# Kernel optimization log

Hardware: AMD Instinct MI355X
Metric: run time of the kernel (lower is better)

## Reference

```python
import jax, jax.numpy as jnp
import numpy as np

M_RANGE = 3
K = 2 * M_RANGE + 1          # kernel size = 7
N_CLASS = K * K              # 49 motion classes
IM_CHANNEL = 3


def setup_inputs() -> dict:
    key = jax.random.key(0)
    k1, k2, k3, k4 = jax.random.split(key, 4)
    B, H, W = 16, 256, 256
    im_input = jax.random.normal(k1, (B, 2 * IM_CHANNEL, H, W), dtype=jnp.float32)
    im_output = jax.random.normal(k2, (B, IM_CHANNEL, H, W), dtype=jnp.float32)
    # motion in [-M_RANGE, M_RANGE-1) so that floor(m)+M_RANGE+1 <= K-1 (valid bin)
    gt_motion = jax.random.uniform(k3, (B, 2, H, W), dtype=jnp.float32) * (2 * M_RANGE - 1) - M_RANGE
    # grouped-conv weight (already in post-swapaxes [n_class, 1, K, K] layout)
    m_kernel = jax.random.uniform(k4, (N_CLASS, 1, K, K), dtype=jnp.float32)
    return {"im_input": im_input, "im_output": im_output,
            "gt_motion": gt_motion, "m_kernel": m_kernel}


def _axis_weights(m):
    # m: [B,H,W] -> bilinear binning weights over K bins: [B,H,W,K]
    f = jnp.floor(m)
    frac = m - f
    idx = f.astype(jnp.int32) + M_RANGE
    oh0 = jax.nn.one_hot(idx, K, dtype=m.dtype)
    oh1 = jax.nn.one_hot(idx + 1, K, dtype=m.dtype)
    return (1.0 - frac)[..., None] * oh0 + frac[..., None] * oh1


def motion2mask(motion):
    # faithful vectorization of the triple-loop: mask[c=iy*K+ix] = b[iy]*a[ix]
    ax = _axis_weights(motion[:, 0])   # x-motion -> columns of ger(b, a)
    ay = _axis_weights(motion[:, 1])   # y-motion -> rows
    mask = ay[..., :, None] * ax[..., None, :]       # [B,H,W,K,K] outer product
    B, H, W = motion.shape[0], motion.shape[2], motion.shape[3]
    return mask.reshape(B, H, W, N_CLASS).transpose(0, 3, 1, 2)  # [B,N_CLASS,H,W]


def _conv(x, w, groups):
    return jax.lax.conv_general_dilated(
        x, w, window_strides=(1, 1),
        padding=[(M_RANGE, M_RANGE), (M_RANGE, M_RANGE)],
        dimension_numbers=("NCHW", "OIHW", "NCHW"),
        feature_group_count=groups)


def reference(im_input, im_output, gt_motion, m_kernel):
    m_mask = motion2mask(gt_motion)                   # [B,N_CLASS,H,W]
    out_mask = _conv(m_mask, m_kernel, N_CLASS)       # grouped conv, same shape
    im = im_input[:, -IM_CHANNEL:]                    # [B,3,H,W]
    B, C, H, W = im.shape
    # construct_image: each channel expanded to N_CLASS copies then grouped-conv
    # == plain conv of each single channel with all N_CLASS kernels
    nearby = _conv(im.reshape(B * C, 1, H, W), m_kernel, 1)
    nearby = nearby.reshape(B, C, N_CLASS, H, W)
    pred = (nearby * out_mask[:, None]).sum(axis=2)   # [B,3,H,W]
    return pred, m_mask
```

## Files before the change

### kernel.cpp

```cpp
#include <hip/hip_runtime.h>
#include <hip/hip_fp16.h>

typedef _Float16 f16x8 __attribute__((ext_vector_type(8)));
typedef float    f32x4 __attribute__((ext_vector_type(4)));

#define TILE   16
#define HALO   22
#define KK     7
#define NCLASS 49
#define IMW    256
#define IMH    256
#define HW     65536
#define HH     484
#define NV     42
#define WROW   34

#define OFF_OMV    0
#define OFF_HALOF  10752
#define OFF_HALOB  11236
#define OFF_KV     11357
#define SH_TOTAL   13415
#define OFF_IML64  10752
#define OFF_IML32  11720

__device__ __forceinline__ unsigned h2u(__half2 h) { union { __half2 h; unsigned u; } c; c.h = h; return c.u; }
__device__ __forceinline__ __half2  u2h(unsigned u) { union { __half2 h; unsigned u; } c; c.u = u; return c.h; }

__global__ __launch_bounds__(256, 3)
void gtnet_kernel(const float* __restrict__ im_input,
                  const float* __restrict__ gt_motion,
                  const float* __restrict__ m_kernel,
                  float* __restrict__ out_pred,
                  float* __restrict__ out_mask)
{
    __shared__ __align__(16) unsigned SH[SH_TOTAL];
    unsigned*      const omV    = SH + OFF_OMV;
    unsigned*      const haloF  = SH + OFF_HALOF;
    unsigned char* const haloB8 = (unsigned char*)(SH + OFF_HALOB);
    unsigned*      const KV     = SH + OFF_KV;
    float2*        const iml64  = (float2*)(SH + OFF_IML64);
    float*         const iml32  = (float*)(SH + OFF_IML32);

    const int tid  = threadIdx.x;
    const int lane = tid & 63, wv_id = tid >> 6;
    const int tx = tid & 15, ty = tid >> 4;
    const int x0 = blockIdx.x * TILE, y0 = blockIdx.y * TILE;
    const int b  = blockIdx.z;
    const int x = x0 + tx, y = y0 + ty;

    const float* mot_x = gt_motion + (size_t)b * 2 * HW;
    const float* mot_y = mot_x + HW;
    const float* imP   = im_input + ((size_t)b * 6 + 3) * HW;

    float2 imr01[2]; float imr2[2];
    #pragma unroll
    for (int k = 0; k < 2; k++) {
        int i = tid + k * 256;
        float2 v01 = make_float2(0.0f, 0.0f); float v2 = 0.0f;
        if (i < HH) {
            int hy = i / HALO, hx = i - hy * HALO;
            int gy = y0 - 3 + hy, gx = x0 - 3 + hx;
            if (gy >= 0 && gy < IMH && gx >= 0 && gx < IMW) {
                int off = gy * IMW + gx;
                v01.x = imP[off];
                v01.y = imP[off + HW];
                v2    = imP[off + 2 * HW];
            }
        }
        imr01[k] = v01; imr2[k] = v2;
    }

    for (int i = tid; i < NCLASS * NV; i += 256) {
        int s = i / NV, n = i - s * NV;
        float k0 = m_kernel[n * NCLASS + s];
        float k7 = m_kernel[(n + KK) * NCLASS + s];
        KV[i] = h2u(__halves2half2(__float2half_rn(k0), __float2half_rn(k7)));
    }
    #pragma unroll
    for (int k = 0; k < 2; k++) {
        int i = tid + k * 256;
        if (i < HH) {
            int hy = i / HALO, hx = i - hy * HALO;
            int gy = y0 - 3 + hy, gx = x0 - 3 + hx;
            unsigned pf = 0u, n4b = 255u;
            if (gy >= 0 && gy < IMH && gx >= 0 && gx < IMW) {
                int off = gy * IMW + gx;
                float ay = mot_y[off] + 3.0f;
                float ax = mot_x[off] + 3.0f;
                float iyf = floorf(ay), ixf = floorf(ax);
                float fy = ay - iyf,    fx = ax - ixf;
                int n00 = (int)iyf * KK + (int)ixf;
                n00 = (n00 < 0) ? 0 : ((n00 > 40) ? 40 : n00);
                pf  = h2u(__halves2half2(__float2half_rn(fy), __float2half_rn(fx)));
                n4b = (unsigned)(n00 * 4);
            }
            haloF[i]  = pf;
            haloB8[i] = (unsigned char)n4b;
        }
    }
    {
        uint4* p = reinterpret_cast<uint4*>(omV);
        for (int i = tid; i < (2 * NV * 128) / 4; i += 256) p[i] = make_uint4(0, 0, 0, 0);
    }

    __syncthreads();

    {
        int off = y * IMW + x;
        float ay = mot_y[off] + 3.0f;
        float ax = mot_x[off] + 3.0f;
        float iyf = floorf(ay), ixf = floorf(ax);
        float fy = ay - iyf,    fx = ax - ixf;
        int   iy = (int)iyf,    ix = (int)ixf;
        float wyA[KK], wxB[KK];
        #pragma unroll
        for (int a = 0; a < KK; a++) {
            wyA[a] = (a == iy) ? (1.0f - fy) : ((a == iy + 1) ? fy : 0.0f);
            wxB[a] = (a == ix) ? (1.0f - fx) : ((a == ix + 1) ? fx : 0.0f);
        }
        float* mm = out_mask + (size_t)b * NCLASS * HW + off;
        #pragma unroll
        for (int a = 0; a < KK; a++)
            #pragma unroll
            for (int bb = 0; bb < KK; bb++)
                mm[(size_t)(a * KK + bb) * HW] = wyA[a] * wxB[bb];
    }

    unsigned* const omHalf = omV + (tid >> 7) * (NV * 128) + (tid & 127);
    const __half hone = __float2half_rn(1.0f);
    #pragma unroll
    for (int u = 0; u < KK; u++) {
        #pragma unroll
        for (int v = 0; v < KK; v++) {
            const int s = u * KK + v;
            const int q = (ty + u) * HALO + (tx + v);
            unsigned pf  = haloF[q];
            unsigned n4u = (unsigned)haloB8[q];
            unsigned n4  = (n4u == 255u) ? 0u : n4u;
            __half2 f2 = u2h(pf);
            __half fy = __low2half(f2), fx = __high2half(f2);
            unsigned wyb = h2u(__halves2half2(__hsub(hone, fy), fy));
            wyb = (n4u == 255u) ? 0u : wyb;
            __half2 wy  = u2h(wyb);
            __half2 wxl = __half2half2(__hsub(hone, fx));
            __half2 wxh = __half2half2(fx);
            const unsigned* kp =
                (const unsigned*)((const char*)KV + s * (NV * 4) + n4);
            unsigned kvA = kp[0], kvB = kp[1];
            unsigned* ob = (unsigned*)((char*)omHalf + n4 * 128);
            unsigned o0 = ob[0], o1 = ob[128];
            __half2 cA = __hmul2(__hmul2(wy, wxl), u2h(kvA));
            __half2 cB = __hmul2(__hmul2(wy, wxh), u2h(kvB));
            ob[0]   = h2u(__hadd2(u2h(o0), cA));
            ob[128] = h2u(__hadd2(u2h(o1), cB));
        }
    }

    __syncthreads();

    #pragma unroll
    for (int k = 0; k < 2; k++) {
        int i = tid + k * 256;
        if (i < HH) { iml64[i] = imr01[k]; iml32[i] = imr2[k]; }
    }

    f32x4 acc[4][4];
    #pragma unroll
    for (int mt = 0; mt < 4; mt++)
        #pragma unroll
        for (int nt = 0; nt < 4; nt++)
            acc[mt][nt] = (f32x4){0.0f, 0.0f, 0.0f, 0.0f};

    const int vb0  = (lane >> 4) * 4;
    const int tcol = lane & 15;
    #pragma unroll
    for (int kit = 0; kit < 3; kit++) {
        f16x8 afk[4];
        #pragma unroll
        for (int mt = 0; mt < 4; mt++) {
            int px = wv_id * 64 + mt * 16 + tcol;
            const unsigned* pxb = omV + (px >> 7) * (NV * 128) + (px & 127);
            int vb = kit * 16 + vb0;
            union { unsigned u[4]; f16x8 v; } au;
            #pragma unroll
            for (int j = 0; j < 4; j++) {
                unsigned d = pxb[(vb + j) * 128];
                au.u[j] = (vb + j <= 41) ? d : 0u;
            }
            afk[mt] = au.v;
        }
        f16x8 bfk[4];
        #pragma unroll
        for (int nt = 0; nt < 4; nt++) {
            int t  = nt * 16 + tcol;
            int tc = (t > 48) ? 48 : t;
            union { unsigned u[4]; f16x8 v; } bu;
            #pragma unroll
            for (int j = 0; j < 4; j++) {
                int v = kit * 16 + vb0 + j;
                float lo = (v <= 41) ? m_kernel[v * NCLASS + tc]        : 0.0f;
                float hi = (v <= 41) ? m_kernel[(v + KK) * NCLASS + tc] : 0.0f;
                bu.u[j] = h2u(__halves2half2(__float2half_rn(lo), __float2half_rn(hi)));
            }
            bfk[nt] = bu.v;
        }
        #pragma unroll
        for (int mt = 0; mt < 4; mt++)
            #pragma unroll
            for (int nt = 0; nt < 4; nt++)
                acc[mt][nt] = __builtin_amdgcn_mfma_f32_16x16x32_f16(afk[mt], bfk[nt], acc[mt][nt], 0, 0, 0);
    }

    __syncthreads();

    #pragma unroll
    for (int mt = 0; mt < 4; mt++) {
        #pragma unroll
        for (int r = 0; r < 4; r++) {
            int px = wv_id * 64 + mt * 16 + (lane >> 4) * 4 + r;
            unsigned* wrow = SH + px * WROW + tcol;
            unsigned v0 = h2u(__halves2half2(__float2half_rn(acc[mt][0][r]),
                                             __float2half_rn(acc[mt][1][r])));
            unsigned v1 = h2u(__halves2half2(__float2half_rn(acc[mt][2][r]),
                                             __float2half_rn(acc[mt][3][r])));
            wrow[0]  = v0;
            wrow[16] = v1;
        }
    }

    __syncthreads();

    union { uint2 q[16]; unsigned d[32]; } wr;
    const uint2* wp = (const uint2*)(SH + tid * WROW);
    #pragma unroll
    for (int c = 0; c < 16; c++) wr.q[c] = wp[c];

    #define WHALF(t) ( (t) < 16 ? __low2half(u2h(wr.d[(t)])) :           \
                       (t) < 32 ? __high2half(u2h(wr.d[(t) - 16])) :     \
                       (t) < 48 ? __low2half(u2h(wr.d[(t) - 16])) :      \
                                  __high2half(u2h(wr.d[16])) )

    float a0 = 0.0f, a1 = 0.0f, a2 = 0.0f;
    #pragma unroll
    for (int p = 0; p < KK; p++) {
        #pragma unroll
        for (int qq = 0; qq < KK; qq++) {
            float wvv = __half2float(WHALF(p * KK + qq));
            int   hq  = (ty + p) * HALO + (tx + qq);
            float2 i01 = iml64[hq];
            float  i2  = iml32[hq];
            a0 = fmaf(wvv, i01.x, a0);
            a1 = fmaf(wvv, i01.y, a1);
            a2 = fmaf(wvv, i2,    a2);
        }
    }
    #undef WHALF
    float* pr = out_pred + (size_t)b * 3 * HW + y * IMW + x;
    pr[0]      = a0;
    pr[HW]     = a1;
    pr[2 * HW] = a2;
}

extern "C" void kernel_launch(void* const* d_in, const int* in_sizes, int n_in,
                              void* d_out, int out_size, void* d_ws, size_t ws_size,
                              hipStream_t stream) {
    const float* im_input  = (const float*)d_in[0];
    const float* gt_motion = (const float*)d_in[2];
    const float* m_kernel  = (const float*)d_in[3];

    float* pred = (float*)d_out;
    float* mask = pred + (size_t)16 * 3 * HW;

    dim3 grid(IMW / TILE, IMH / TILE, 16);
    dim3 block(256);
    hipLaunchKernelGGL(gtnet_kernel, grid, block, 0, stream,
                       im_input, gt_motion, m_kernel, pred, mask);
}
```

Baseline: 336.7 us.

## Precompute packed fp16 kernel operands in a setup kernel, use packed-math asm

A small setup kernel now converts m_kernel into packed fp16 MFMA B-fragments and the KV table in workspace once per launch. The main kernel loads them with vectorized uint4 copies instead of recomputing scattered fp32 gathers and conversions in every block. The motion-weight splat uses inline v_pk_fma/v_pk_mul with op_sel to cut scalar half ops, and halo loads are hoisted per row. This adds a second launch and extra global traffic for the precomputed tables, and holds B fragments in registers, which raises register pressure.

```diff
diff --git a/kernel.cpp b/kernel.cpp
--- a/kernel.cpp
+++ b/kernel.cpp
@@ -18,20 +18,54 @@
 #define OFF_OMV    0
 #define OFF_HALOF  10752
 #define OFF_HALOB  11236
-#define OFF_KV     11357
-#define SH_TOTAL   13415
+#define OFF_KV     11360
+#define SH_TOTAL   13424
 #define OFF_IML64  10752
 #define OFF_IML32  11720
 
+#define WS_B    0
+#define WS_KV   3072
+#define WS_KV4  (3072/4)
+
 __device__ __forceinline__ unsigned h2u(__half2 h) { union { __half2 h; unsigned u; } c; c.h = h; return c.u; }
 __device__ __forceinline__ __half2  u2h(unsigned u) { union { __half2 h; unsigned u; } c; c.u = u; return c.h; }
+
+__global__ void gtnet_setup(const float* __restrict__ m_kernel, unsigned* __restrict__ ws)
+{
+    const int tid = threadIdx.x;
+    for (int idx = tid; idx < 768; idx += 256) {
+        int lane = idx & 63, kitnt = idx >> 6;
+        int kit = kitnt >> 2, nt = kitnt & 3;
+        int vb0 = (lane >> 4) * 4, tcol = lane & 15;
+        int t = nt * 16 + tcol; int tc = (t > 48) ? 48 : t;
+        uint4 o;
+        unsigned* op = (unsigned*)&o;
+        #pragma unroll
+        for (int j = 0; j < 4; j++) {
+            int v = kit * 16 + vb0 + j;
+            float lo = (v <= 41) ? m_kernel[v * NCLASS + tc]        : 0.0f;
+            float hi = (v <= 41) ? m_kernel[(v + KK) * NCLASS + tc] : 0.0f;
+            op[j] = h2u(__halves2half2(__float2half_rn(lo), __float2half_rn(hi)));
+        }
+        ((uint4*)ws)[idx] = o;
+    }
+    for (int i = tid; i < 2064; i += 256) {
+        unsigned val = 0u;
+        if (i < NCLASS * NV) {
+            int s = i / NV, n = i - s * NV;
+            val = h2u(__halves2half2(__float2half_rn(m_kernel[n * NCLASS + s]),
+                                     __float2half_rn(m_kernel[(n + KK) * NCLASS + s])));
+        }
+        ws[WS_KV + i] = val;
+    }
+}
 
 __global__ __launch_bounds__(256, 3)
 void gtnet_kernel(const float* __restrict__ im_input,
                   const float* __restrict__ gt_motion,
-                  const float* __restrict__ m_kernel,
                   float* __restrict__ out_pred,
-                  float* __restrict__ out_mask)
+                  float* __restrict__ out_mask,
+                  const unsigned* __restrict__ ws)
 {
     __shared__ __align__(16) unsigned SH[SH_TOTAL];
     unsigned*      const omV    = SH + OFF_OMV;
@@ -70,11 +104,10 @@
         imr01[k] = v01; imr2[k] = v2;
     }
 
-    for (int i = tid; i < NCLASS * NV; i += 256) {
-        int s = i / NV, n = i - s * NV;
-        float k0 = m_kernel[n * NCLASS + s];
-        float k7 = m_kernel[(n + KK) * NCLASS + s];
-        KV[i] = h2u(__halves2half2(__float2half_rn(k0), __float2half_rn(k7)));
+    {
+        const uint4* kvsrc = (const uint4*)(ws + WS_KV);
+        uint4*       kvdst = (uint4*)KV;
+        for (int i = tid; i < 516; i += 256) kvdst[i] = kvsrc[i];
     }
     #pragma unroll
     for (int k = 0; k < 2; k++) {
@@ -127,36 +160,56 @@
     }
 
     unsigned* const omHalf = omV + (tid >> 7) * (NV * 128) + (tid & 127);
-    const __half hone = __float2half_rn(1.0f);
+    const unsigned c_m11 = 0x3C00BC00u;
+    const unsigned c_10  = 0x00003C00u;
     #pragma unroll
     for (int u = 0; u < KK; u++) {
+        unsigned pfr[KK], n4r[KK];
+        #pragma unroll
+        for (int v = 0; v < KK; v++) {
+            int q = (ty + u) * HALO + (tx + v);
+            pfr[v] = haloF[q];
+            n4r[v] = (unsigned)haloB8[q];
+        }
         #pragma unroll
         for (int v = 0; v < KK; v++) {
             const int s = u * KK + v;
-            const int q = (ty + u) * HALO + (tx + v);
-            unsigned pf  = haloF[q];
-            unsigned n4u = (unsigned)haloB8[q];
+            unsigned n4u = n4r[v];
             unsigned n4  = (n4u == 255u) ? 0u : n4u;
-            __half2 f2 = u2h(pf);
-            __half fy = __low2half(f2), fx = __high2half(f2);
-            unsigned wyb = h2u(__halves2half2(__hsub(hone, fy), fy));
+            unsigned wyb, wx2;
+            asm("v_pk_fma_f16 %0, %1, %2, %3 op_sel:[0,0,0] op_sel_hi:[0,1,1]"
+                : "=v"(wyb) : "v"(pfr[v]), "v"(c_m11), "v"(c_10));
+            asm("v_pk_fma_f16 %0, %1, %2, %3 op_sel:[1,0,0] op_sel_hi:[1,1,1]"
+                : "=v"(wx2) : "v"(pfr[v]), "v"(c_m11), "v"(c_10));
             wyb = (n4u == 255u) ? 0u : wyb;
-            __half2 wy  = u2h(wyb);
-            __half2 wxl = __half2half2(__hsub(hone, fx));
-            __half2 wxh = __half2half2(fx);
             const unsigned* kp =
                 (const unsigned*)((const char*)KV + s * (NV * 4) + n4);
             unsigned kvA = kp[0], kvB = kp[1];
             unsigned* ob = (unsigned*)((char*)omHalf + n4 * 128);
             unsigned o0 = ob[0], o1 = ob[128];
-            __half2 cA = __hmul2(__hmul2(wy, wxl), u2h(kvA));
-            __half2 cB = __hmul2(__hmul2(wy, wxh), u2h(kvB));
+            unsigned tA, tB;
+            asm("v_pk_mul_f16 %0, %1, %2 op_sel:[0,0] op_sel_hi:[1,0]"
+                : "=v"(tA) : "v"(wyb), "v"(wx2));
+            asm("v_pk_mul_f16 %0, %1, %2 op_sel:[0,1] op_sel_hi:[1,1]"
+                : "=v"(tB) : "v"(wyb), "v"(wx2));
+            __half2 cA = __hmul2(u2h(tA), u2h(kvA));
+            __half2 cB = __hmul2(u2h(tB), u2h(kvB));
             ob[0]   = h2u(__hadd2(u2h(o0), cA));
             ob[128] = h2u(__hadd2(u2h(o1), cB));
         }
     }
 
     __syncthreads();
+
+    uint4 braw[3][4];
+    {
+        const uint4* bsrc = (const uint4*)(ws + WS_B);
+        #pragma unroll
+        for (int kit = 0; kit < 3; kit++)
+            #pragma unroll
+            for (int nt = 0; nt < 4; nt++)
+                braw[kit][nt] = bsrc[(kit * 4 + nt) * 64 + lane];
+    }
 
     #pragma unroll
     for (int k = 0; k < 2; k++) {
@@ -189,26 +242,14 @@
             }
             afk[mt] = au.v;
         }
-        f16x8 bfk[4];
-        #pragma unroll
-        for (int nt = 0; nt < 4; nt++) {
-            int t  = nt * 16 + tcol;
-            int tc = (t > 48) ? 48 : t;
-            union { unsigned u[4]; f16x8 v; } bu;
+        #pragma unroll
+        for (int mt = 0; mt < 4; mt++) {
             #pragma unroll
-            for (int j = 0; j < 4; j++) {
-                int v = kit * 16 + vb0 + j;
-                float lo = (v <= 41) ? m_kernel[v * NCLASS + tc]        : 0.0f;
-                float hi = (v <= 41) ? m_kernel[(v + KK) * NCLASS + tc] : 0.0f;
-                bu.u[j] = h2u(__halves2half2(__float2half_rn(lo), __float2half_rn(hi)));
+            for (int nt = 0; nt < 4; nt++) {
+                union { uint4 q; f16x8 v; } bc; bc.q = braw[kit][nt];
+                acc[mt][nt] = __builtin_amdgcn_mfma_f32_16x16x32_f16(afk[mt], bc.v, acc[mt][nt], 0, 0, 0);
             }
-            bfk[nt] = bu.v;
-        }
-        #pragma unroll
-        for (int mt = 0; mt < 4; mt++)
-            #pragma unroll
-            for (int nt = 0; nt < 4; nt++)
-                acc[mt][nt] = __builtin_amdgcn_mfma_f32_16x16x32_f16(afk[mt], bfk[nt], acc[mt][nt], 0, 0, 0);
+        }
     }
 
     __syncthreads();
@@ -271,8 +312,11 @@
     float* pred = (float*)d_out;
     float* mask = pred + (size_t)16 * 3 * HW;
 
+    hipLaunchKernelGGL(gtnet_setup, dim3(1), dim3(256), 0, stream,
+                       m_kernel, (unsigned*)d_ws);
+
     dim3 grid(IMW / TILE, IMH / TILE, 16);
     dim3 block(256);
     hipLaunchKernelGGL(gtnet_kernel, grid, block, 0, stream,
-                       im_input, gt_motion, m_kernel, pred, mask);
+                       im_input, gt_motion, pred, mask, (const unsigned*)d_ws);
 }
```

New measurement: 329.3 us. 1.02x faster.
